# Performance work log

Measured on AMD Instinct MI355X. Metric: run time of the kernel, lower is better.

Reference implementation:

```python
import jax, jax.numpy as jnp
import numpy as np

EMBED_DIM = 1024
NUM_HEADS = 32
MULT = 2                      # edit_channel_multiply_factor
HPM = NUM_HEADS // MULT       # heads_per_multiply = 16
HEAD_DIM = EMBED_DIM * MULT // NUM_HEADS  # 64


def setup_inputs() -> dict:
    key = jax.random.key(0)
    ks = jax.random.split(key, 8)
    B, Q, S, D = 8, 4096, 128, EMBED_DIM
    return {
        "encoder_hidden_states": jax.random.normal(ks[0], (B, Q, D), dtype=jnp.float32),
        "hidden_states": jax.random.normal(ks[1], (B, S, D), dtype=jnp.float32),
        # Conv1D weights are [nx, nf] (input-major, like GPT-2), std=0.02; biases zero
        "q_w": jax.random.normal(ks[2], (MULT, D, D), dtype=jnp.float32) * 0.02,
        "q_b": jnp.zeros((MULT, D), dtype=jnp.float32),
        "c_attn_w": jax.random.normal(ks[3], (MULT, D, 2 * D), dtype=jnp.float32) * 0.02,
        "c_attn_b": jnp.zeros((MULT, 2 * D), dtype=jnp.float32),
        "c_proj_w": jax.random.normal(ks[4], (MULT, D, D), dtype=jnp.float32) * 0.02,
        "c_proj_b": jnp.zeros((MULT, D), dtype=jnp.float32),
    }


def _forward(encoder_hidden_states, hidden_states, q_w, q_b,
             c_attn_w, c_attn_b, c_proj_w, c_proj_b):
    B, Q, D = encoder_hidden_states.shape
    # last-token hidden state supplies K/V (kv_len == 1)
    h_last = hidden_states[:, -1, :]                                  # [B, D]

    # all M projections batched via einsum over the multiply dim 'm'
    q = jnp.einsum("bqe,mef->mbqf", encoder_hidden_states, q_w) \
        + q_b[:, None, None, :]                                       # [M, B, Q, D]
    kv = jnp.einsum("be,mef->mbf", h_last, c_attn_w) \
        + c_attn_b[:, None, :]                                        # [M, B, 2D]
    k, v = kv[..., :D], kv[..., D:]                                   # [M, B, D]

    # split heads: D = HPM * HEAD_DIM
    q = q.reshape(MULT, B, Q, HPM, HEAD_DIM)                          # [M,B,Q,H,d]
    k = k.reshape(MULT, B, HPM, HEAD_DIM)                             # [M,B,H,d]
    v = v.reshape(MULT, B, HPM, HEAD_DIM)

    # GPT2 eager attention with a single key: scores [M,B,H,Q] (kv=1)
    scores = jnp.einsum("mbqhd,mbhd->mbhq", q, k) / jnp.sqrt(
        jnp.asarray(HEAD_DIM, dtype=q.dtype))
    # softmax over the kv axis (size 1) -> identically 1, kept for fidelity
    w = jax.nn.softmax(scores[..., None], axis=-1)                    # [M,B,H,Q,1]
    attn = w * v[:, :, :, None, :]                                    # [M,B,H,Q,d]

    # merge heads -> [M, B, Q, D], then output projection
    attn = attn.transpose(0, 1, 3, 2, 4).reshape(MULT, B, Q, D)
    out_m = jnp.einsum("mbqd,mde->mbqe", attn, c_proj_w) \
        + c_proj_b[:, None, None, :]                                  # [M,B,Q,D]

    # faithful accumulation: outputs[0][0] += attn_output[0] for i > 0
    # (only batch element 0 receives contributions from multiplies > 0)
    out = out_m[0]
    out = out.at[0].add(jnp.sum(out_m[1:, 0], axis=0))
    return out


def reference(encoder_hidden_states, hidden_states, q_w, q_b,
              c_attn_w, c_attn_b, c_proj_w, c_proj_b):
    return _forward(encoder_hidden_states, hidden_states, q_w, q_b,
                    c_attn_w, c_attn_b, c_proj_w, c_proj_b)
```

## Files before the change

kernel.cpp:

```cpp
#include <hip/hip_runtime.h>

#define DIM    1024
#define BATCH  8
#define QLEN   4096
#define SEQ    128
#define NMULT  2
#define ESPLIT 16
#define DCHUNK (DIM / ESPLIT)

typedef float vfloat4 __attribute__((ext_vector_type(4)));

__global__ void __launch_bounds__(256) fused_gemv(const float* __restrict__ hidden,
                                                  const float* __restrict__ c_attn_w,
                                                  const float* __restrict__ c_attn_b,
                                                  const float* __restrict__ c_proj_w,
                                                  float* __restrict__ yp) {
    __shared__ float h_lds[DIM];
    __shared__ float vred[4][DCHUNK];
    __shared__ float v_lds[DCHUNK];

    int m = blockIdx.x >> 7;
    int b = (blockIdx.x >> 4) & 7;
    int c = blockIdx.x & 15;
    int tid = threadIdx.x;

    const vfloat4* h4 = reinterpret_cast<const vfloat4*>(
        hidden + (size_t)b * (SEQ * DIM) + (size_t)(SEQ - 1) * DIM);
    reinterpret_cast<vfloat4*>(h_lds)[tid] = h4[tid];
    __syncthreads();

    int eg = tid >> 6;
    int dl = tid & 63;
    int dbase = c * DCHUNK;
    const float* wv = c_attn_w + (size_t)m * DIM * (2 * DIM) + DIM + dbase + dl;
    float acc = 0.f;
#pragma unroll 8
    for (int e = eg; e < DIM; e += 4) {
        acc += h_lds[e] * wv[(size_t)e * (2 * DIM)];
    }
    vred[eg][dl] = acc;
    __syncthreads();
    if (tid < DCHUNK) {
        v_lds[tid] = vred[0][tid] + vred[1][tid] + vred[2][tid] + vred[3][tid]
                   + c_attn_b[m * 2 * DIM + DIM + dbase + tid];
    }
    __syncthreads();

    const float* wp = c_proj_w + (size_t)m * DIM * DIM + (size_t)dbase * DIM + 4 * tid;
    vfloat4 acc2 = {0.f, 0.f, 0.f, 0.f};
#pragma unroll 8
    for (int d = 0; d < DCHUNK; ++d) {
        float vd = v_lds[d];
        vfloat4 w4 = *reinterpret_cast<const vfloat4*>(wp + (size_t)d * DIM);
        acc2 += vd * w4;
    }
    float* dst = yp + (((m * BATCH + b) * ESPLIT) + c) * DIM + 4 * tid;
    *reinterpret_cast<vfloat4*>(dst) = acc2;
}

__global__ void __launch_bounds__(256) bcast_reduce(const float* __restrict__ yp,
                                                    const float* __restrict__ c_proj_b,
                                                    float* __restrict__ out) {
    int b = blockIdx.x >> 8;
    int q0 = (blockIdx.x & 255) * 16;
    int t = threadIdx.x;

    const vfloat4* bias0 = reinterpret_cast<const vfloat4*>(c_proj_b);
    vfloat4 val = bias0[t];
    const vfloat4* base0 = reinterpret_cast<const vfloat4*>(
        yp + (size_t)(0 * BATCH + b) * ESPLIT * DIM) + t;
#pragma unroll
    for (int c = 0; c < ESPLIT; ++c) {
        val += base0[c * (DIM / 4)];
    }
    if (b == 0) {
        vfloat4 v1 = bias0[DIM / 4 + t];
        const vfloat4* base1 = reinterpret_cast<const vfloat4*>(
            yp + (size_t)(1 * BATCH + 0) * ESPLIT * DIM) + t;
#pragma unroll
        for (int c = 0; c < ESPLIT; ++c) {
            v1 += base1[c * (DIM / 4)];
        }
        val += v1;
    }

    vfloat4* o = reinterpret_cast<vfloat4*>(out)
               + ((size_t)b * QLEN + q0) * (DIM / 4) + t;
#pragma unroll
    for (int q = 0; q < 16; ++q) {
        __builtin_nontemporal_store(val, o + (size_t)q * (DIM / 4));
    }
}

extern "C" void kernel_launch(void* const* d_in, const int* in_sizes, int n_in,
                              void* d_out, int out_size, void* d_ws, size_t ws_size,
                              hipStream_t stream) {
    const float* hidden   = (const float*)d_in[1];
    const float* c_attn_w = (const float*)d_in[4];
    const float* c_attn_b = (const float*)d_in[5];
    const float* c_proj_w = (const float*)d_in[6];
    const float* c_proj_b = (const float*)d_in[7];
    float* out = (float*)d_out;

    float* yp = (float*)d_ws;

    fused_gemv<<<NMULT * BATCH * ESPLIT, 256, 0, stream>>>(hidden, c_attn_w,
                                                           c_attn_b, c_proj_w, yp);
    bcast_reduce<<<2048, 256, 0, stream>>>(yp, c_proj_b, out);
}
```

Measured before the change: 43.78 us.

## Batch all batch elements per weight tile in split-K two-stage GEMV

```diff
diff --git a/kernel.cpp b/kernel.cpp
--- a/kernel.cpp
+++ b/kernel.cpp
@@ -5,57 +5,109 @@
 #define QLEN   4096
 #define SEQ    128
 #define NMULT  2
-#define ESPLIT 16
-#define DCHUNK (DIM / ESPLIT)
 
 typedef float vfloat4 __attribute__((ext_vector_type(4)));
 
-__global__ void __launch_bounds__(256) fused_gemv(const float* __restrict__ hidden,
-                                                  const float* __restrict__ c_attn_w,
-                                                  const float* __restrict__ c_attn_b,
-                                                  const float* __restrict__ c_proj_w,
-                                                  float* __restrict__ yp) {
-    __shared__ float h_lds[DIM];
-    __shared__ float vred[4][DCHUNK];
-    __shared__ float v_lds[DCHUNK];
+__global__ void __launch_bounds__(256) kernelA(const float* __restrict__ hidden,
+                                               const float* __restrict__ c_attn_w,
+                                               float* __restrict__ vp) {
+    __shared__ float h_s[BATCH][64];
+    __shared__ vfloat4 vred[16][16][9];
 
-    int m = blockIdx.x >> 7;
-    int b = (blockIdx.x >> 4) & 7;
-    int c = blockIdx.x & 15;
-    int tid = threadIdx.x;
+    const int tid = threadIdx.x;
+    const int es = blockIdx.x & 15;
+    const int c  = (blockIdx.x >> 4) & 15;
+    const int m  = blockIdx.x >> 8;
 
-    const vfloat4* h4 = reinterpret_cast<const vfloat4*>(
-        hidden + (size_t)b * (SEQ * DIM) + (size_t)(SEQ - 1) * DIM);
-    reinterpret_cast<vfloat4*>(h_lds)[tid] = h4[tid];
-    __syncthreads();
-
-    int eg = tid >> 6;
-    int dl = tid & 63;
-    int dbase = c * DCHUNK;
-    const float* wv = c_attn_w + (size_t)m * DIM * (2 * DIM) + DIM + dbase + dl;
-    float acc = 0.f;
-#pragma unroll 8
-    for (int e = eg; e < DIM; e += 4) {
-        acc += h_lds[e] * wv[(size_t)e * (2 * DIM)];
-    }
-    vred[eg][dl] = acc;
-    __syncthreads();
-    if (tid < DCHUNK) {
-        v_lds[tid] = vred[0][tid] + vred[1][tid] + vred[2][tid] + vred[3][tid]
-                   + c_attn_b[m * 2 * DIM + DIM + dbase + tid];
+    if (tid < 128) {
+        int b = tid >> 4, e4 = tid & 15;
+        const vfloat4* src = reinterpret_cast<const vfloat4*>(
+            hidden + (size_t)b * (SEQ * DIM) + (size_t)(SEQ - 1) * DIM + es * 64);
+        reinterpret_cast<vfloat4*>(h_s[b])[e4] = src[e4];
     }
     __syncthreads();
 
-    const float* wp = c_proj_w + (size_t)m * DIM * DIM + (size_t)dbase * DIM + 4 * tid;
-    vfloat4 acc2 = {0.f, 0.f, 0.f, 0.f};
-#pragma unroll 8
-    for (int d = 0; d < DCHUNK; ++d) {
-        float vd = v_lds[d];
-        vfloat4 w4 = *reinterpret_cast<const vfloat4*>(wp + (size_t)d * DIM);
-        acc2 += vd * w4;
+    const int d4 = tid & 15;
+    const int eg = tid >> 4;
+    const float* wbase = c_attn_w + (size_t)m * DIM * (2 * DIM) + DIM + c * 64 + d4 * 4;
+
+    vfloat4 acc[BATCH];
+#pragma unroll
+    for (int b = 0; b < BATCH; ++b) acc[b] = (vfloat4){0.f, 0.f, 0.f, 0.f};
+
+#pragma unroll
+    for (int k = 0; k < 4; ++k) {
+        int el = eg * 4 + k;
+        int e  = es * 64 + el;
+        vfloat4 w4 = *reinterpret_cast<const vfloat4*>(wbase + (size_t)e * (2 * DIM));
+#pragma unroll
+        for (int b = 0; b < BATCH; ++b) acc[b] += h_s[b][el] * w4;
     }
-    float* dst = yp + (((m * BATCH + b) * ESPLIT) + c) * DIM + 4 * tid;
-    *reinterpret_cast<vfloat4*>(dst) = acc2;
+#pragma unroll
+    for (int b = 0; b < BATCH; ++b) vred[eg][d4][b] = acc[b];
+    __syncthreads();
+
+    if (tid < 128) {
+        int b = tid >> 4, dq = tid & 15;
+        vfloat4 s = vred[0][dq][b];
+#pragma unroll
+        for (int g = 1; g < 16; ++g) s += vred[g][dq][b];
+        reinterpret_cast<vfloat4*>(vp)[es * 4096 + (m * BATCH + b) * 256 + c * 16 + dq] = s;
+    }
+}
+
+__global__ void __launch_bounds__(256) kernelB(const float* __restrict__ vp,
+                                               const float* __restrict__ c_attn_b,
+                                               const float* __restrict__ c_proj_w,
+                                               float* __restrict__ yp) {
+    __shared__ float v_s[BATCH][64];
+    __shared__ vfloat4 yred[16][16][9];
+
+    const int tid = threadIdx.x;
+    const int ce = blockIdx.x & 15;
+    const int cd = (blockIdx.x >> 4) & 15;
+    const int m  = blockIdx.x >> 8;
+
+    if (tid < 128) {
+        int b = tid >> 4, d4 = tid & 15;
+        vfloat4 s = reinterpret_cast<const vfloat4*>(
+            c_attn_b + (size_t)m * 2 * DIM + DIM)[cd * 16 + d4];
+        const vfloat4* vp4 = reinterpret_cast<const vfloat4*>(vp);
+#pragma unroll
+        for (int es = 0; es < 16; ++es) {
+            s += vp4[es * 4096 + (m * BATCH + b) * 256 + cd * 16 + d4];
+        }
+        reinterpret_cast<vfloat4*>(v_s[b])[d4] = s;
+    }
+    __syncthreads();
+
+    const int e4 = tid & 15;
+    const int dg = tid >> 4;
+    const float* wbase = c_proj_w + (size_t)m * DIM * DIM + ce * 64 + e4 * 4;
+
+    vfloat4 acc[BATCH];
+#pragma unroll
+    for (int b = 0; b < BATCH; ++b) acc[b] = (vfloat4){0.f, 0.f, 0.f, 0.f};
+
+#pragma unroll
+    for (int j = 0; j < 4; ++j) {
+        int dl = dg * 4 + j;
+        int d  = cd * 64 + dl;
+        vfloat4 w4 = *reinterpret_cast<const vfloat4*>(wbase + (size_t)d * DIM);
+#pragma unroll
+        for (int b = 0; b < BATCH; ++b) acc[b] += v_s[b][dl] * w4;
+    }
+#pragma unroll
+    for (int b = 0; b < BATCH; ++b) yred[dg][e4][b] = acc[b];
+    __syncthreads();
+
+    if (tid < 128) {
+        int b = tid >> 4, eq = tid & 15;
+        vfloat4 s = yred[0][eq][b];
+#pragma unroll
+        for (int g = 1; g < 16; ++g) s += yred[g][eq][b];
+        reinterpret_cast<vfloat4*>(yp)[cd * 4096 + (m * BATCH + b) * 256 + ce * 16 + eq] = s;
+    }
 }
 
 __global__ void __launch_bounds__(256) bcast_reduce(const float* __restrict__ yp,
@@ -65,30 +117,25 @@
     int q0 = (blockIdx.x & 255) * 16;
     int t = threadIdx.x;
 
-    const vfloat4* bias0 = reinterpret_cast<const vfloat4*>(c_proj_b);
-    vfloat4 val = bias0[t];
-    const vfloat4* base0 = reinterpret_cast<const vfloat4*>(
-        yp + (size_t)(0 * BATCH + b) * ESPLIT * DIM) + t;
+    const vfloat4* bias4 = reinterpret_cast<const vfloat4*>(c_proj_b);
+    const vfloat4* yp4 = reinterpret_cast<const vfloat4*>(yp);
+    vfloat4 val = bias4[t];
 #pragma unroll
-    for (int c = 0; c < ESPLIT; ++c) {
-        val += base0[c * (DIM / 4)];
+    for (int cd = 0; cd < 16; ++cd) {
+        val += yp4[cd * 4096 + b * 256 + t];
     }
     if (b == 0) {
-        vfloat4 v1 = bias0[DIM / 4 + t];
-        const vfloat4* base1 = reinterpret_cast<const vfloat4*>(
-            yp + (size_t)(1 * BATCH + 0) * ESPLIT * DIM) + t;
+        val += bias4[256 + t];
 #pragma unroll
-        for (int c = 0; c < ESPLIT; ++c) {
-            v1 += base1[c * (DIM / 4)];
+        for (int cd = 0; cd < 16; ++cd) {
+            val += yp4[cd * 4096 + BATCH * 256 + t];
         }
-        val += v1;
     }
 
-    vfloat4* o = reinterpret_cast<vfloat4*>(out)
-               + ((size_t)b * QLEN + q0) * (DIM / 4) + t;
+    vfloat4* o = reinterpret_cast<vfloat4*>(out) + ((size_t)b * QLEN + q0) * 256 + t;
 #pragma unroll
     for (int q = 0; q < 16; ++q) {
-        __builtin_nontemporal_store(val, o + (size_t)q * (DIM / 4));
+        __builtin_nontemporal_store(val, o + (size_t)q * 256);
     }
 }
 
@@ -102,9 +149,10 @@
     const float* c_proj_b = (const float*)d_in[7];
     float* out = (float*)d_out;
 
-    float* yp = (float*)d_ws;
+    float* vp = (float*)d_ws;
+    float* yp = vp + 16 * 16384;
 
-    fused_gemv<<<NMULT * BATCH * ESPLIT, 256, 0, stream>>>(hidden, c_attn_w,
-                                                           c_attn_b, c_proj_w, yp);
+    kernelA<<<512, 256, 0, stream>>>(hidden, c_attn_w, vp);
+    kernelB<<<512, 256, 0, stream>>>(vp, c_attn_b, c_proj_w, yp);
     bcast_reduce<<<2048, 256, 0, stream>>>(yp, c_proj_b, out);
 }
```

Result: faster. 37.96 us (-13.3%).
